# Kernel optimization log

Hardware: AMD Instinct MI355X
Metric: run time of the kernel (lower is better)

The kernel has to match this reference:

```python
import jax, jax.numpy as jnp
import numpy as np

B, T, C, HD = 8, 2048, 1024, 64  # batch, seq, feature_size, head_dim = C // n_head


def setup_inputs() -> dict:
    key = jax.random.key(0)
    kx, kq, kk, kv = jax.random.split(key, 4)
    return {
        "x": jax.random.normal(kx, (B, T, C), dtype=jnp.float32),
        "Wq": jax.random.normal(kq, (C, HD), dtype=jnp.float32) * 0.02,
        "Wk": jax.random.normal(kk, (C, HD), dtype=jnp.float32) * 0.02,
        "Wv": jax.random.normal(kv, (C, HD), dtype=jnp.float32) * 0.02,
    }


def reference(x, Wq, Wk, Wv):
    # x: [B, T, C]; W*: [C, HD] (Linear(feature_size, feature_size//n_head, bias=False))
    Bsz, Tlen, Cdim = x.shape
    q = x @ Wq  # [B, T, HD]
    k = x @ Wk
    v = x @ Wv
    scores = jnp.einsum("btd,bsd->bts", q, k)  # [B, T, T]
    causal = jnp.tril(jnp.ones((Tlen, Tlen), dtype=bool))
    # faithful to source: masked_fill(-inf) THEN divide by sqrt(C) (full feature size)
    scores = jnp.where(causal, scores, -jnp.inf) / jnp.sqrt(jnp.float32(Cdim))
    att = jax.nn.softmax(scores, axis=-1)  # dropout p=0.0 (eval) -> identity
    return att @ v  # [B, T, HD]
```

## Files before the change

kernel.cpp:

```cpp
#include <hip/hip_runtime.h>


#define BATCH 8
#define SEQ   2048
#define CIN   1024
#define HDIM  64
#define NROW  (BATCH * SEQ)
#define NQT   (NROW / 16)
#define UNITS 576

typedef __attribute__((ext_vector_type(8))) short bf16x8;
typedef __attribute__((ext_vector_type(4))) short u16x4;
typedef __attribute__((ext_vector_type(4))) float f32x4;

__device__ __forceinline__ unsigned short f2bf(float f) {
  unsigned int u = __builtin_bit_cast(unsigned int, f);
  u += 0x7fffu + ((u >> 16) & 1u);
  return (unsigned short)(u >> 16);
}
__device__ __forceinline__ float bf2f(unsigned short h) {
  return __builtin_bit_cast(float, (unsigned int)h << 16);
}
__device__ __forceinline__ u16x4 pack4(f32x4 a) {
  u16x4 r;
  r[0] = (short)f2bf(a[0]); r[1] = (short)f2bf(a[1]);
  r[2] = (short)f2bf(a[2]); r[3] = (short)f2bf(a[3]);
  return r;
}

__global__ __launch_bounds__(256) void wtrans_k(const float* __restrict__ wq,
                                                const float* __restrict__ wk,
                                                const float* __restrict__ wv,
                                                unsigned short* __restrict__ wt) {
  __shared__ unsigned short lds[64][65];
  const int m  = blockIdx.x >> 4;
  const int c0 = (blockIdx.x & 15) * 64;
  const float* w = (m == 0) ? wq : (m == 1) ? wk : wv;
  const int nl = threadIdx.x & 63, gr = threadIdx.x >> 6;
#pragma unroll
  for (int i = 0; i < 16; ++i) {
    int cl = gr * 16 + i;
    lds[cl][nl] = f2bf(w[(size_t)(c0 + cl) * HDIM + nl]);
  }
  __syncthreads();
#pragma unroll
  for (int i = 0; i < 16; ++i) {
    int n = gr * 16 + i;
    wt[(size_t)m * 65536 + n * CIN + c0 + nl] = lds[nl][n];
  }
}

__global__ __launch_bounds__(512) void qkv_proj_k(const float* __restrict__ x,
                                                  const unsigned short* __restrict__ wt,
                                                  unsigned short* __restrict__ q,
                                                  unsigned short* __restrict__ k,
                                                  unsigned short* __restrict__ vt) {
  __shared__ __align__(16) unsigned char ldsb[28672];
  const int tid  = threadIdx.x;
  const int lane = tid & 63;
  const int w    = tid >> 6;
  const int lr   = lane & 15, lg = lane >> 4;
  const int wm   = w & 1, wn = w >> 1;
  const int row0 = blockIdx.x * 32;

  const int trow  = tid >> 4;
  const int tcol4 = (tid & 15) * 4;
  const float* xg = x + (size_t)(row0 + trow) * CIN + tcol4;
  const int xoff  = trow * 128 + (((tcol4 >> 3) ^ (trow & 7)) << 4) + ((tcol4 & 4) << 1);

  const int wrow_ = tid >> 3;
  const int wg8   = tid & 7;
  const unsigned short* wg[3];
  int woff[3];
#pragma unroll
  for (int c = 0; c < 3; ++c) {
    int wrow = c * 64 + wrow_;
    wg[c]   = wt + (size_t)wrow * CIN + wg8 * 8;
    woff[c] = 4096 + wrow * 128 + ((wg8 ^ (wrow & 7)) << 4);
  }

  f32x4 acc[3];
#pragma unroll
  for (int i = 0; i < 3; ++i) acc[i] = (f32x4){0.f, 0.f, 0.f, 0.f};

  const int arow_off = (wm * 16 + lr) * 128;
  const int brow0    = wn * 48 + lr;

#pragma unroll 1
  for (int t = 0; t < 16; ++t) {
    const int k0 = t * 64;
    f32x4 xv = *(const f32x4*)(xg + k0);
    bf16x8 w0 = *(const bf16x8*)(wg[0] + k0);
    bf16x8 w1 = *(const bf16x8*)(wg[1] + k0);
    bf16x8 w2 = *(const bf16x8*)(wg[2] + k0);
    __syncthreads();
    *(u16x4*)(void*)(ldsb + xoff)    = pack4(xv);
    *(bf16x8*)(void*)(ldsb + woff[0]) = w0;
    *(bf16x8*)(void*)(ldsb + woff[1]) = w1;
    *(bf16x8*)(void*)(ldsb + woff[2]) = w2;
    __syncthreads();
#pragma unroll
    for (int kk = 0; kk < 2; ++kk) {
      const int swz = (((kk << 2) | lg) ^ (lr & 7)) << 4;
      bf16x8 af = *(const bf16x8*)(void*)(ldsb + arow_off + swz);
#pragma unroll
      for (int f = 0; f < 3; ++f) {
        bf16x8 bf_ = *(const bf16x8*)(void*)(ldsb + 4096 + (brow0 + f * 16) * 128 + swz);
        acc[f] = __builtin_amdgcn_mfma_f32_16x16x32_bf16(af, bf_, acc[f], 0, 0, 0);
      }
    }
  }

#pragma unroll
  for (int f = 0; f < 3; ++f) {
    const int gc  = wn * 48 + f * 16;
    const int mat = gc >> 6;
    const int hd  = (gc & 63) + lr;
#pragma unroll
    for (int j = 0; j < 4; ++j) {
      int grow = row0 + wm * 16 + lg * 4 + j;
      float v = acc[f][j];
      if (mat == 0) {
        q[(size_t)grow * HDIM + hd] = f2bf(v * 0.03125f);
      } else if (mat == 1) {
        k[(size_t)grow * HDIM + hd] = f2bf(v);
      } else {
        int b = grow >> 11, tp = grow & 2047;
        vt[((size_t)b * HDIM + hd) * SEQ + tp] = f2bf(v);
      }
    }
  }
}

__global__ __launch_bounds__(256) void attn_k(const unsigned short* __restrict__ q,
                                              const unsigned short* __restrict__ k,
                                              const unsigned short* __restrict__ vt,
                                              float* __restrict__ opart,
                                              float* __restrict__ m_l) {
  __shared__ __align__(16) unsigned short plds[4][16][72];
  const int lane = threadIdx.x & 63;
  const int w    = threadIdx.x >> 6;
  const int lr = lane & 15, lg = lane >> 4;
  const int u    = blockIdx.x * 4 + w;
  const int b    = u / UNITS;
  const int unit = u - b * UNITS;
  int a = 0;
#pragma unroll
  for (int i = 0; i < 7; ++i) if (8 * (a + 1) * (a + 2) <= unit) ++a;
  const int S    = a + 1;
  const int rem  = unit - 8 * a * S;
  const int qt   = 16 * a + rem / S;
  const int seg  = rem - (rem / S) * S;
  const int row0 = qt * 16;
  const int p    = b * UNITS + unit;
  unsigned short (*pw)[72] = plds[w];

  const unsigned short* qb_ = q  + (size_t)b * SEQ * HDIM;
  const unsigned short* kb_ = k  + (size_t)b * SEQ * HDIM;
  const unsigned short* vb_ = vt + (size_t)b * HDIM * SEQ;

  bf16x8 qf0 = *(const bf16x8*)(qb_ + (row0 + lr) * HDIM + lg * 8);
  bf16x8 qf1 = *(const bf16x8*)(qb_ + (row0 + lr) * HDIM + 32 + lg * 8);

  f32x4 o[4];
#pragma unroll
  for (int n = 0; n < 4; ++n) o[n] = (f32x4){0.f, 0.f, 0.f, 0.f};
  float m_run = -INFINITY, l_run = 0.f;
  const int   qrow = row0 + lr;
  const float LOG2E = 1.44269504f;
  const int nt = (qt >> 2) + 1;
  const int lo = (nt * seg) / S;
  const int hi = (nt * (seg + 1)) / S;

  for (int t = lo; t < hi; ++t) {
    const int kv = t * 64;
    f32x4 sv[4];
#pragma unroll
    for (int f = 0; f < 4; ++f) {
      bf16x8 ka0 = *(const bf16x8*)(kb_ + (kv + f * 16 + lr) * HDIM + lg * 8);
      bf16x8 ka1 = *(const bf16x8*)(kb_ + (kv + f * 16 + lr) * HDIM + 32 + lg * 8);
      sv[f] = (f32x4){0.f, 0.f, 0.f, 0.f};
      sv[f] = __builtin_amdgcn_mfma_f32_16x16x32_bf16(ka0, qf0, sv[f], 0, 0, 0);
      sv[f] = __builtin_amdgcn_mfma_f32_16x16x32_bf16(ka1, qf1, sv[f], 0, 0, 0);
    }
    if (kv + 63 > row0) {
#pragma unroll
      for (int f = 0; f < 4; ++f)
#pragma unroll
        for (int j = 0; j < 4; ++j)
          if (kv + f * 16 + lg * 4 + j > qrow) sv[f][j] = -INFINITY;
    }
    float tm = -INFINITY;
#pragma unroll
    for (int f = 0; f < 4; ++f)
#pragma unroll
      for (int j = 0; j < 4; ++j) tm = fmaxf(tm, sv[f][j]);
    tm = fmaxf(tm, __shfl_xor(tm, 16, 64));
    tm = fmaxf(tm, __shfl_xor(tm, 32, 64));
    float m_new = fmaxf(m_run, tm);
    float alpha = (m_run == -INFINITY) ? 0.f : exp2f((m_run - m_new) * LOG2E);
    float mc    = (m_new == -INFINITY) ? 0.f : m_new * LOG2E;
    float ps = 0.f;
#pragma unroll
    for (int f = 0; f < 4; ++f) {
      float p0 = exp2f(sv[f][0] * LOG2E - mc);
      float p1 = exp2f(sv[f][1] * LOG2E - mc);
      float p2 = exp2f(sv[f][2] * LOG2E - mc);
      float p3 = exp2f(sv[f][3] * LOG2E - mc);
      ps += (p0 + p1) + (p2 + p3);
      unsigned int lo32 = (unsigned int)f2bf(p0) | ((unsigned int)f2bf(p1) << 16);
      unsigned int hi32 = (unsigned int)f2bf(p2) | ((unsigned int)f2bf(p3) << 16);
      uint2 pk; pk.x = lo32; pk.y = hi32;
      *(uint2*)(&pw[lr][f * 16 + lg * 4]) = pk;
    }
    ps += __shfl_xor(ps, 16, 64);
    ps += __shfl_xor(ps, 32, 64);
    l_run = l_run * alpha + ps;
    m_run = m_new;
#pragma unroll
    for (int j = 0; j < 4; ++j) {
      float aj = __shfl(alpha, lg * 4 + j, 64);
      o[0][j] *= aj; o[1][j] *= aj; o[2][j] *= aj; o[3][j] *= aj;
    }
    asm volatile("s_waitcnt lgkmcnt(0)" ::: "memory");
    __builtin_amdgcn_sched_barrier(0);
#pragma unroll
    for (int kk = 0; kk < 2; ++kk) {
      bf16x8 pf = *(const bf16x8*)(&pw[lr][kk * 32 + lg * 8]);
#pragma unroll
      for (int n = 0; n < 4; ++n) {
        bf16x8 vf = *(const bf16x8*)(vb_ + (n * 16 + lr) * SEQ + kv + kk * 32 + lg * 8);
        o[n] = __builtin_amdgcn_mfma_f32_16x16x32_bf16(pf, vf, o[n], 0, 0, 0);
      }
    }
  }

  if (lane < 16) {
    m_l[p * 32 + lane]      = m_run;
    m_l[p * 32 + 16 + lane] = l_run;
  }
#pragma unroll
  for (int j = 0; j < 4; ++j) {
    int r = lg * 4 + j;
#pragma unroll
    for (int n = 0; n < 4; ++n)
      opart[(size_t)p * 1024 + r * 64 + n * 16 + lr] = o[n][j];
  }
}

__global__ __launch_bounds__(256) void combine_k(const float* __restrict__ opart,
                                                 const float* __restrict__ m_l,
                                                 float* __restrict__ out) {
  const float LOG2E = 1.44269504f;
  int idx = blockIdx.x * 256 + threadIdx.x;
  int col = idx & 63;
  int row = idx >> 6;
  int b = row >> 11, t = row & 2047;
  int qt = t >> 4, r = t & 15;
  int a = qt >> 4;
  int S = a + 1;
  int pb = b * UNITS + 8 * a * S + (qt & 15) * S;
  float M = -INFINITY;
  for (int s = 0; s < S; ++s) M = fmaxf(M, m_l[(pb + s) * 32 + r]);
  float l = 0.f, o = 0.f;
  for (int s = 0; s < S; ++s) {
    float ms = m_l[(pb + s) * 32 + r];
    float w  = exp2f((ms - M) * LOG2E);
    l += m_l[(pb + s) * 32 + 16 + r] * w;
    o += opart[(size_t)(pb + s) * 1024 + r * 64 + col] * w;
  }
  out[(size_t)row * HDIM + col] = o / l;
}

extern "C" void kernel_launch(void* const* d_in, const int* in_sizes, int n_in,
                              void* d_out, int out_size, void* d_ws, size_t ws_size,
                              hipStream_t stream) {
  const float* x  = (const float*)d_in[0];
  const float* wq = (const float*)d_in[1];
  const float* wk = (const float*)d_in[2];
  const float* wv = (const float*)d_in[3];
  float* outp = (float*)d_out;

  const int NP = BATCH * UNITS;
  float* m_l   = (float*)d_ws;
  float* opart = m_l + (size_t)NP * 32;
  unsigned short* qbuf = (unsigned short*)(opart + (size_t)NP * 1024);
  unsigned short* kbuf = qbuf + (size_t)NROW * HDIM;
  unsigned short* vbuf = kbuf + (size_t)NROW * HDIM;
  unsigned short* wt   = vbuf + (size_t)NROW * HDIM;

  hipLaunchKernelGGL(wtrans_k, dim3(48), dim3(256), 0, stream, wq, wk, wv, wt);
  hipLaunchKernelGGL(qkv_proj_k, dim3(NROW / 32), dim3(512), 0, stream, x, wt, qbuf, kbuf, vbuf);
  hipLaunchKernelGGL(attn_k, dim3(NP / 4), dim3(256), 0, stream, qbuf, kbuf, vbuf, opart, m_l);
  hipLaunchKernelGGL(combine_k, dim3(NROW * HDIM / 256), dim3(256), 0, stream, opart, m_l, outp);
}
```

Baseline: 169.2 us.

## Share 128-key K/V tiles in LDS across 8 waves per attention block

Restructures the split-KV attention so each 512-thread block handles a 128-row query tile against one 128-key segment. K and V are staged once into XOR-swizzled LDS and shared by all eight waves, where previously each wave read them directly from global memory. The intent is to cut redundant global/L2 traffic and improve reuse. In exchange there are more partial results (a 128-row opart per block), the combine kernel reads more partials, and each block gets only two inner iterations, leaving little latency hiding.

```diff
diff --git a/kernel.cpp b/kernel.cpp
--- a/kernel.cpp
+++ b/kernel.cpp
@@ -6,8 +6,8 @@
 #define CIN   1024
 #define HDIM  64
 #define NROW  (BATCH * SEQ)
-#define NQT   (NROW / 16)
-#define UNITS 576
+#define UPB   136
+#define NPB   (BATCH * UPB)
 
 typedef __attribute__((ext_vector_type(8))) short bf16x8;
 typedef __attribute__((ext_vector_type(4))) short u16x4;
@@ -132,58 +132,76 @@
   }
 }
 
-__global__ __launch_bounds__(256) void attn_k(const unsigned short* __restrict__ q,
+__global__ __launch_bounds__(512) void attn_k(const unsigned short* __restrict__ q,
                                               const unsigned short* __restrict__ k,
                                               const unsigned short* __restrict__ vt,
                                               float* __restrict__ opart,
                                               float* __restrict__ m_l) {
-  __shared__ __align__(16) unsigned short plds[4][16][72];
-  const int lane = threadIdx.x & 63;
-  const int w    = threadIdx.x >> 6;
-  const int lr = lane & 15, lg = lane >> 4;
-  const int u    = blockIdx.x * 4 + w;
-  const int b    = u / UNITS;
-  const int unit = u - b * UNITS;
-  int a = 0;
-#pragma unroll
-  for (int i = 0; i < 7; ++i) if (8 * (a + 1) * (a + 2) <= unit) ++a;
-  const int S    = a + 1;
-  const int rem  = unit - 8 * a * S;
-  const int qt   = 16 * a + rem / S;
-  const int seg  = rem - (rem / S) * S;
-  const int row0 = qt * 16;
-  const int p    = b * UNITS + unit;
-  unsigned short (*pw)[72] = plds[w];
+  __shared__ __align__(16) unsigned char kv_lds[4][8192];
+  __shared__ __align__(16) unsigned short plds[8][16][72];
+  const int tid  = threadIdx.x;
+  const int lane = tid & 63;
+  const int w    = tid >> 6;
+  const int lr = lane & 15, lg = lane >> 4, lr7 = lane & 7;
+
+  const int blk = blockIdx.x;
+  const int b   = blk / UPB;
+  const int u   = blk - b * UPB;
+  int i = 0;
+#pragma unroll
+  for (int j = 1; j <= 15; ++j) if (((j * (j + 1)) >> 1) <= u) i = j;
+  const int seg  = u - ((i * (i + 1)) >> 1);
+  const int r0   = i * 128 + w * 16;
+  const int kvb  = seg * 128;
+  const int p    = blk;
 
   const unsigned short* qb_ = q  + (size_t)b * SEQ * HDIM;
   const unsigned short* kb_ = k  + (size_t)b * SEQ * HDIM;
   const unsigned short* vb_ = vt + (size_t)b * HDIM * SEQ;
 
-  bf16x8 qf0 = *(const bf16x8*)(qb_ + (row0 + lr) * HDIM + lg * 8);
-  bf16x8 qf1 = *(const bf16x8*)(qb_ + (row0 + lr) * HDIM + 32 + lg * 8);
+  const int srow = tid >> 3;
+  const int sg   = tid & 7;
+  const unsigned short* ks0 = kb_ + (size_t)(kvb + srow) * HDIM + sg * 8;
+  const unsigned short* vs0 = vb_ + (size_t)srow * SEQ + kvb + sg * 8;
+  bf16x8 kv0 = *(const bf16x8*)(ks0);
+  bf16x8 vv0 = *(const bf16x8*)(vs0);
+  bf16x8 kv1 = *(const bf16x8*)(ks0 + 64 * HDIM);
+  bf16x8 vv1 = *(const bf16x8*)(vs0 + 64);
+  bf16x8 qf0 = *(const bf16x8*)(qb_ + (size_t)(r0 + lr) * HDIM + lg * 8);
+  bf16x8 qf1 = *(const bf16x8*)(qb_ + (size_t)(r0 + lr) * HDIM + 32 + lg * 8);
+  const int soff = srow * 128 + ((sg ^ (srow & 7)) << 4);
+  *(bf16x8*)(kv_lds[0] + soff) = kv0;
+  *(bf16x8*)(kv_lds[1] + soff) = vv0;
+  *(bf16x8*)(kv_lds[2] + soff) = kv1;
+  *(bf16x8*)(kv_lds[3] + soff) = vv1;
+  __syncthreads();
 
   f32x4 o[4];
 #pragma unroll
   for (int n = 0; n < 4; ++n) o[n] = (f32x4){0.f, 0.f, 0.f, 0.f};
   float m_run = -INFINITY, l_run = 0.f;
-  const int   qrow = row0 + lr;
+  const int   qrow = r0 + lr;
   const float LOG2E = 1.44269504f;
-  const int nt = (qt >> 2) + 1;
-  const int lo = (nt * seg) / S;
-  const int hi = (nt * (seg + 1)) / S;
-
-  for (int t = lo; t < hi; ++t) {
-    const int kv = t * 64;
+  unsigned short (*pw)[72] = plds[w];
+
+#pragma unroll 1
+  for (int tt = 0; tt < 2; ++tt) {
+    const int kv = kvb + tt * 64;
+    if (kv > r0 + 15) continue;
+    const unsigned char* Kt = kv_lds[tt * 2];
+    const unsigned char* Vt = kv_lds[tt * 2 + 1];
+
     f32x4 sv[4];
 #pragma unroll
     for (int f = 0; f < 4; ++f) {
-      bf16x8 ka0 = *(const bf16x8*)(kb_ + (kv + f * 16 + lr) * HDIM + lg * 8);
-      bf16x8 ka1 = *(const bf16x8*)(kb_ + (kv + f * 16 + lr) * HDIM + 32 + lg * 8);
+      const int base = (f * 16 + lr) * 128;
+      bf16x8 ka0 = *(const bf16x8*)(Kt + base + ((lg ^ lr7) << 4));
+      bf16x8 ka1 = *(const bf16x8*)(Kt + base + (((4 + lg) ^ lr7) << 4));
       sv[f] = (f32x4){0.f, 0.f, 0.f, 0.f};
       sv[f] = __builtin_amdgcn_mfma_f32_16x16x32_bf16(ka0, qf0, sv[f], 0, 0, 0);
       sv[f] = __builtin_amdgcn_mfma_f32_16x16x32_bf16(ka1, qf1, sv[f], 0, 0, 0);
     }
-    if (kv + 63 > row0) {
+    if (kv + 63 > r0) {
 #pragma unroll
       for (int f = 0; f < 4; ++f)
 #pragma unroll
@@ -229,22 +247,22 @@
       bf16x8 pf = *(const bf16x8*)(&pw[lr][kk * 32 + lg * 8]);
 #pragma unroll
       for (int n = 0; n < 4; ++n) {
-        bf16x8 vf = *(const bf16x8*)(vb_ + (n * 16 + lr) * SEQ + kv + kk * 32 + lg * 8);
+        bf16x8 vf = *(const bf16x8*)(Vt + (n * 16 + lr) * 128 + (((kk * 4 + lg) ^ lr7) << 4));
         o[n] = __builtin_amdgcn_mfma_f32_16x16x32_bf16(pf, vf, o[n], 0, 0, 0);
       }
     }
   }
 
   if (lane < 16) {
-    m_l[p * 32 + lane]      = m_run;
-    m_l[p * 32 + 16 + lane] = l_run;
+    m_l[p * 256 + w * 16 + lane]       = m_run;
+    m_l[p * 256 + 128 + w * 16 + lane] = l_run;
   }
 #pragma unroll
   for (int j = 0; j < 4; ++j) {
-    int r = lg * 4 + j;
+    int rloc = w * 16 + lg * 4 + j;
 #pragma unroll
     for (int n = 0; n < 4; ++n)
-      opart[(size_t)p * 1024 + r * 64 + n * 16 + lr] = o[n][j];
+      opart[(size_t)p * 8192 + rloc * 64 + n * 16 + lr] = o[n][j];
   }
 }
 
@@ -256,18 +274,17 @@
   int col = idx & 63;
   int row = idx >> 6;
   int b = row >> 11, t = row & 2047;
-  int qt = t >> 4, r = t & 15;
-  int a = qt >> 4;
-  int S = a + 1;
-  int pb = b * UNITS + 8 * a * S + (qt & 15) * S;
+  int i = t >> 7, r = t & 127;
+  int S = i + 1;
+  int pb = b * UPB + ((i * (i + 1)) >> 1);
   float M = -INFINITY;
-  for (int s = 0; s < S; ++s) M = fmaxf(M, m_l[(pb + s) * 32 + r]);
+  for (int s = 0; s < S; ++s) M = fmaxf(M, m_l[(pb + s) * 256 + r]);
   float l = 0.f, o = 0.f;
   for (int s = 0; s < S; ++s) {
-    float ms = m_l[(pb + s) * 32 + r];
+    float ms = m_l[(pb + s) * 256 + r];
     float w  = exp2f((ms - M) * LOG2E);
-    l += m_l[(pb + s) * 32 + 16 + r] * w;
-    o += opart[(size_t)(pb + s) * 1024 + r * 64 + col] * w;
+    l += m_l[(pb + s) * 256 + 128 + r] * w;
+    o += opart[(size_t)(pb + s) * 8192 + r * 64 + col] * w;
   }
   out[(size_t)row * HDIM + col] = o / l;
 }
@@ -281,16 +298,15 @@
   const float* wv = (const float*)d_in[3];
   float* outp = (float*)d_out;
 
-  const int NP = BATCH * UNITS;
   float* m_l   = (float*)d_ws;
-  float* opart = m_l + (size_t)NP * 32;
-  unsigned short* qbuf = (unsigned short*)(opart + (size_t)NP * 1024);
+  float* opart = m_l + (size_t)NPB * 256;
+  unsigned short* qbuf = (unsigned short*)(opart + (size_t)NPB * 8192);
   unsigned short* kbuf = qbuf + (size_t)NROW * HDIM;
   unsigned short* vbuf = kbuf + (size_t)NROW * HDIM;
   unsigned short* wt   = vbuf + (size_t)NROW * HDIM;
 
   hipLaunchKernelGGL(wtrans_k, dim3(48), dim3(256), 0, stream, wq, wk, wv, wt);
   hipLaunchKernelGGL(qkv_proj_k, dim3(NROW / 32), dim3(512), 0, stream, x, wt, qbuf, kbuf, vbuf);
-  hipLaunchKernelGGL(attn_k, dim3(NP / 4), dim3(256), 0, stream, qbuf, kbuf, vbuf, opart, m_l);
+  hipLaunchKernelGGL(attn_k, dim3(NPB), dim3(512), 0, stream, qbuf, kbuf, vbuf, opart, m_l);
   hipLaunchKernelGGL(combine_k, dim3(NROW * HDIM / 256), dim3(256), 0, stream, opart, m_l, outp);
 }
```

After: 151.4 us. 1.12x faster.
